# Optimization experiments

Hardware: AMD Instinct MI355X
Metric: run time of the kernel (lower is better)

## Reference

```python
import jax, jax.numpy as jnp
import numpy as np

N, N1, N2, E, DIN, H = 100000, 60000, 30000, 1600000, 128, 64


def setup_inputs() -> dict:
    key = jax.random.key(0)
    ks = jax.random.split(key, 16)
    s = 0.05
    return {
        "feats0": jax.random.normal(ks[0], (N, DIN), jnp.float32),
        "feats1": jax.random.normal(ks[1], (N1, DIN), jnp.float32),
        "feats2": jax.random.normal(ks[2], (N2, DIN), jnp.float32),
        "mask_feat": jax.random.normal(ks[3], (N, DIN), jnp.float32),
        "src1": jax.random.randint(ks[4], (E,), 0, N, jnp.int32),
        "dst1": jax.random.randint(ks[5], (E,), 0, N1, jnp.int32),
        "src2": jax.random.randint(ks[6], (E,), 0, N, jnp.int32),
        "dst2": jax.random.randint(ks[7], (E,), 0, N2, jnp.int32),
        "W0": jax.random.normal(ks[8], (DIN, H), jnp.float32) * s,
        "b0": jnp.zeros((H,), jnp.float32),
        "W1": jax.random.normal(ks[9], (DIN, H), jnp.float32) * s,
        "b1": jnp.zeros((H,), jnp.float32),
        "W2": jax.random.normal(ks[10], (DIN, H), jnp.float32) * s,
        "b2": jnp.zeros((H,), jnp.float32),
        "A0": jax.random.normal(ks[11], (H, H), jnp.float32) * s,
        "A1": jax.random.normal(ks[12], (H, H), jnp.float32) * s,
    }


def _mean_agg(h_nei, src, dst, num_tar):
    # sparse mm(nei_index, h_nei) / count  ==  degree-normalized neighbor mean
    summed = jax.ops.segment_sum(h_nei[dst], src, num_segments=num_tar)
    cnt = jax.ops.segment_sum(jnp.ones(src.shape, h_nei.dtype), src, num_segments=num_tar)
    cnt = jnp.where(cnt > 0, cnt, 1.0)[:, None]  # torch.where(count>0, count, 1)
    return summed / cnt


def reference(feats0, feats1, feats2, mask_feat, src1, dst1, src2, dst2,
              W0, b0, W1, b1, W2, b2, A0, A1):
    elu = jax.nn.elu
    h_tar = elu(feats0 @ W0 + b0)
    h_mask = elu(mask_feat @ W0 + b0)
    h_nei1 = elu(feats1 @ W1 + b1)
    h_nei2 = elu(feats2 @ W2 + b2)

    agg1 = _mean_agg(h_nei1, src1, dst1, feats0.shape[0]) @ A0
    agg2 = _mean_agg(h_nei2, src2, dst2, feats0.shape[0]) @ A1

    view1 = elu(h_tar + agg1)
    mask1 = elu(h_mask + agg1)
    view2 = elu(h_tar + agg2)
    mask2 = elu(h_mask + agg2)
    # [5, N, H]: per-relation view/mask embeddings plus coarse target embedding
    return jnp.stack([view1, mask1, view2, mask2, h_tar])
```

## Files before the change

kernel.cpp:

```cpp
#include <hip/hip_runtime.h>
#include <hip/hip_bf16.h>


typedef short  bf16x8 __attribute__((ext_vector_type(8)));
typedef float  f32x4  __attribute__((ext_vector_type(4)));
typedef int    i32x4  __attribute__((ext_vector_type(4)));

#define MFMA_BF16(a, b, c) __builtin_amdgcn_mfma_f32_16x16x32_bf16((a), (b), (c), 0, 0, 0)

__device__ __forceinline__ ushort f2bf(float f) {
  return (ushort)((__float_as_uint(f) + 0x8000u) >> 16);
}
__device__ __forceinline__ float eluf(float x) {
  return x > 0.f ? x : (__expf(x) - 1.f);
}
__device__ __forceinline__ bf16x8 cvt8(const float* __restrict__ p) {
  f32x4 lo = *(const f32x4*)p;
  f32x4 hi = *(const f32x4*)(p + 4);
  union { unsigned u[4]; bf16x8 v; } r;
#pragma unroll
  for (int j = 0; j < 2; ++j) {
    unsigned a = __float_as_uint(lo[2 * j])     + 0x8000u;
    unsigned b = __float_as_uint(lo[2 * j + 1]) + 0x8000u;
    r.u[j] = (a >> 16) | (b & 0xFFFF0000u);
    unsigned c = __float_as_uint(hi[2 * j])     + 0x8000u;
    unsigned d = __float_as_uint(hi[2 * j + 1]) + 0x8000u;
    r.u[2 + j] = (c >> 16) | (d & 0xFFFF0000u);
  }
  return r.v;
}

__global__ __launch_bounds__(256) void pack_frags_kernel(
    const float* __restrict__ W0, const float* __restrict__ W1,
    const float* __restrict__ W2, const float* __restrict__ A0,
    const float* __restrict__ A1, ushort* __restrict__ out) {
  int gw   = (blockIdx.x * blockDim.x + threadIdx.x) >> 6;
  int lane = threadIdx.x & 63;
  if (gw >= 64) return;
  const float* src; ushort* dst; int f;
  if (gw < 16)      { src = W0; dst = out;         f = gw;      }
  else if (gw < 32) { src = W1; dst = out + 8192;  f = gw - 16; }
  else if (gw < 48) { src = W2; dst = out + 16384; f = gw - 32; }
  else if (gw < 56) { src = A0; dst = out + 24576; f = gw - 48; }
  else              { src = A1; dst = out + 28672; f = gw - 56; }
  int kc = f >> 2, ct = f & 3;
  int q = lane >> 4, c = lane & 15;
  ushort* d = dst + ((size_t)f * 64 + lane) * 8;
#pragma unroll
  for (int i = 0; i < 8; ++i)
    d[i] = f2bf(src[(kc * 32 + q * 8 + i) * 64 + ct * 16 + c]);
}

template <bool HASA>
__global__ __launch_bounds__(256) void lin_elu_kernel(
    const float* __restrict__ X, const ushort* __restrict__ Wp,
    const float* __restrict__ bias, const ushort* __restrict__ Ap,
    float* __restrict__ Y, int Mtiles) {
  __shared__ ushort plds[4][16 * 72];
  int lane  = threadIdx.x & 63;
  int q     = lane >> 4, c = lane & 15;
  int wslot = threadIdx.x >> 6;
  int wid   = blockIdx.x * 4 + wslot;
  int nw    = gridDim.x * 4;

  bf16x8 bw[4][4];
#pragma unroll
  for (int kc = 0; kc < 4; ++kc)
#pragma unroll
    for (int ct = 0; ct < 4; ++ct)
      bw[kc][ct] = *(const bf16x8*)(Wp + (((kc << 2) | ct) * 64 + lane) * 8);

  float bv[4];
#pragma unroll
  for (int ct = 0; ct < 4; ++ct) bv[ct] = bias[ct * 16 + c];

  bf16x8 ba[2][4];
  if (HASA) {
#pragma unroll
    for (int kc = 0; kc < 2; ++kc)
#pragma unroll
      for (int ct = 0; ct < 4; ++ct)
        ba[kc][ct] = *(const bf16x8*)(Ap + (((kc << 2) | ct) * 64 + lane) * 8);
  }

  ushort* myp = plds[wslot];

  for (int t = wid; t < Mtiles; t += nw) {
    const float* xr = X + ((size_t)(t * 16 + c)) * 128 + q * 8;
    bf16x8 a0 = cvt8(xr);
    bf16x8 a1 = cvt8(xr + 32);
    bf16x8 a2 = cvt8(xr + 64);
    bf16x8 a3 = cvt8(xr + 96);

    f32x4 acc[4];
#pragma unroll
    for (int ct = 0; ct < 4; ++ct) {
      f32x4 a = {0.f, 0.f, 0.f, 0.f};
      a = MFMA_BF16(a0, bw[0][ct], a);
      a = MFMA_BF16(a1, bw[1][ct], a);
      a = MFMA_BF16(a2, bw[2][ct], a);
      a = MFMA_BF16(a3, bw[3][ct], a);
      acc[ct] = a;
    }

    float* yr = Y + ((size_t)t * 16) * 64;
    if (!HASA) {
#pragma unroll
      for (int ct = 0; ct < 4; ++ct)
#pragma unroll
        for (int r = 0; r < 4; ++r)
          yr[(q * 4 + r) * 64 + ct * 16 + c] = eluf(acc[ct][r] + bv[ct]);
    } else {
#pragma unroll
      for (int ct = 0; ct < 4; ++ct)
#pragma unroll
        for (int r = 0; r < 4; ++r)
          myp[(q * 4 + r) * 72 + ct * 16 + c] = f2bf(eluf(acc[ct][r] + bv[ct]));
      bf16x8 p0 = *(const bf16x8*)(myp + c * 72 + q * 8);
      bf16x8 p1 = *(const bf16x8*)(myp + c * 72 + 32 + q * 8);
      f32x4 acc2[4];
#pragma unroll
      for (int ct = 0; ct < 4; ++ct) {
        f32x4 a = {0.f, 0.f, 0.f, 0.f};
        a = MFMA_BF16(p0, ba[0][ct], a);
        a = MFMA_BF16(p1, ba[1][ct], a);
        acc2[ct] = a;
      }
#pragma unroll
      for (int ct = 0; ct < 4; ++ct)
#pragma unroll
        for (int r = 0; r < 4; ++r)
          yr[(q * 4 + r) * 64 + ct * 16 + c] = acc2[ct][r];
    }
  }
}

__global__ __launch_bounds__(256) void bucket_count_kernel(
    const int* __restrict__ src1, const int* __restrict__ src2,
    int* __restrict__ btot, int E, int N) {
  __shared__ int h[256];
  int t = threadIdx.x;
  h[t] = 0;
  __syncthreads();
  int n4 = (2 * E) >> 2;
  int stride = gridDim.x * blockDim.x;
  for (int i = blockIdx.x * blockDim.x + t; i < n4; i += stride) {
    int e4 = i << 2;
    i32x4 k;
    if (e4 < E) k = *(const i32x4*)(src1 + e4);
    else {
      k = *(const i32x4*)(src2 + (e4 - E));
#pragma unroll
      for (int j = 0; j < 4; ++j) k[j] += N;
    }
#pragma unroll
    for (int j = 0; j < 4; ++j) atomicAdd(&h[k[j] >> 10], 1);
  }
  __syncthreads();
  if (h[t]) atomicAdd(&btot[t], h[t]);
}

__global__ __launch_bounds__(256) void bscan_kernel(
    const int* __restrict__ btot, int* __restrict__ bstart,
    int* __restrict__ bcur, int NB) {
  __shared__ int lds[256];
  int t = threadIdx.x;
  int v = (t < NB) ? btot[t] : 0;
  lds[t] = v; __syncthreads();
  for (int off = 1; off < 256; off <<= 1) {
    int x = lds[t];
    int a = (t >= off) ? lds[t - off] : 0;
    __syncthreads();
    lds[t] = x + a;
    __syncthreads();
  }
  int incl = lds[t];
  if (t < NB) { bstart[t] = incl - v; bcur[t] = incl - v; }
  if (t == NB - 1) bstart[NB] = incl;
}

#define P1_CHUNK 8192
__global__ __launch_bounds__(256) void partition_kernel(
    const int* __restrict__ src1, const int* __restrict__ dst1,
    const int* __restrict__ src2, const int* __restrict__ dst2,
    int* __restrict__ bcur, unsigned* __restrict__ pairs, int E, int N) {
  __shared__ int hist[256], sbuf[256], lbase[256], lcur[256], gstart[256];
  __shared__ unsigned img[P1_CHUNK];
  int t  = threadIdx.x;
  int M  = 2 * N;
  int NB = (M + 1023) >> 10;
  int cb = blockIdx.x * P1_CHUNK;
  int ng = (2 * E - cb) >> 2;
  if (ng > P1_CHUNK / 4) ng = P1_CHUNK / 4;

  hist[t] = 0;
  __syncthreads();

  for (int i = t; i < ng; i += 256) {
    int e4 = cb + (i << 2);
    i32x4 k;
    if (e4 < E) k = *(const i32x4*)(src1 + e4);
    else {
      k = *(const i32x4*)(src2 + (e4 - E));
#pragma unroll
      for (int j = 0; j < 4; ++j) k[j] += N;
    }
#pragma unroll
    for (int j = 0; j < 4; ++j) atomicAdd(&hist[k[j] >> 10], 1);
  }
  __syncthreads();

  sbuf[t] = hist[t];
  __syncthreads();
  for (int off = 1; off < 256; off <<= 1) {
    int x = sbuf[t];
    int a = (t >= off) ? sbuf[t - off] : 0;
    __syncthreads();
    sbuf[t] = x + a;
    __syncthreads();
  }
  lbase[t] = sbuf[t] - hist[t];
  lcur[t]  = sbuf[t] - hist[t];
  if (t < NB) gstart[t] = atomicAdd(&bcur[t], hist[t]);
  __syncthreads();

  for (int i = t; i < ng; i += 256) {
    int e4 = cb + (i << 2);
    i32x4 k, v;
    if (e4 < E) {
      k = *(const i32x4*)(src1 + e4);
      v = *(const i32x4*)(dst1 + e4);
    } else {
      k = *(const i32x4*)(src2 + (e4 - E));
      v = *(const i32x4*)(dst2 + (e4 - E));
#pragma unroll
      for (int j = 0; j < 4; ++j) k[j] += N;
    }
#pragma unroll
    for (int j = 0; j < 4; ++j) {
      int b  = k[j] >> 10;
      int lp = atomicAdd(&lcur[b], 1);
      img[lp] = ((unsigned)(k[j] & 1023) << 16) | (unsigned)v[j];
    }
  }
  __syncthreads();

  int w = t >> 6, lane = t & 63;
  for (int b = w; b < NB; b += 4) {
    int len = hist[b], lb = lbase[b], gs = gstart[b];
    for (int i = lane; i < len; i += 64)
      pairs[gs + i] = img[lb + i];
  }
}

#define P2_CAP 18432
__global__ __launch_bounds__(256) void scatter_kernel(
    const int* __restrict__ bstart, const unsigned* __restrict__ pairs,
    int* __restrict__ row_ptr, int* __restrict__ nbr, int M) {
  __shared__ int cur[1024];
  __shared__ int ssum[256];
  __shared__ int img[P2_CAP];
  int t     = threadIdx.x;
  int b     = blockIdx.x;
  int kbase = b << 10;
  int kend  = kbase + 1024; if (kend > M) kend = M;
  int kcnt  = kend - kbase;
  int pbase = bstart[b];
  int cnt   = bstart[b + 1] - pbase;

#pragma unroll
  for (int j = 0; j < 4; ++j) cur[t * 4 + j] = 0;
  __syncthreads();
  for (int i = t; i < cnt; i += 256)
    atomicAdd(&cur[pairs[pbase + i] >> 16], 1);
  __syncthreads();

  int c0 = cur[t * 4], c1 = cur[t * 4 + 1], c2 = cur[t * 4 + 2], c3 = cur[t * 4 + 3];
  int s  = c0 + c1 + c2 + c3;
  ssum[t] = s;
  __syncthreads();
  for (int off = 1; off < 256; off <<= 1) {
    int x = ssum[t];
    int a = (t >= off) ? ssum[t - off] : 0;
    __syncthreads();
    ssum[t] = x + a;
    __syncthreads();
  }
  int run = ssum[t] - s;
  int e0 = run, e1 = run + c0, e2 = e1 + c1, e3 = e2 + c2;
  cur[t * 4] = e0; cur[t * 4 + 1] = e1; cur[t * 4 + 2] = e2; cur[t * 4 + 3] = e3;
  if (t * 4 + 3 < kcnt) {
    i32x4 rp = { pbase + e0, pbase + e1, pbase + e2, pbase + e3 };
    *(i32x4*)(row_ptr + kbase + t * 4) = rp;
  } else {
    if (t * 4     < kcnt) row_ptr[kbase + t * 4]     = pbase + e0;
    if (t * 4 + 1 < kcnt) row_ptr[kbase + t * 4 + 1] = pbase + e1;
    if (t * 4 + 2 < kcnt) row_ptr[kbase + t * 4 + 2] = pbase + e2;
    if (t * 4 + 3 < kcnt) row_ptr[kbase + t * 4 + 3] = pbase + e3;
  }
  if (t == 0 && kend == M) row_ptr[M] = pbase + cnt;
  __syncthreads();

  for (int i = t; i < cnt; i += 256) {
    unsigned p = pairs[pbase + i];
    int kl = (int)(p >> 16);
    int v  = (int)(p & 0xFFFFu);
    int pos = atomicAdd(&cur[kl], 1);
    if (pos < P2_CAP) img[pos] = v;
    else              nbr[pbase + pos] = v;
  }
  __syncthreads();

  int lim = cnt < P2_CAP ? cnt : P2_CAP;
  for (int i = t; i < lim; i += 256) nbr[pbase + i] = img[i];
}

__global__ __launch_bounds__(256) void aggregate_kernel(
    const int* __restrict__ row_ptr, const int* __restrict__ nbr,
    const float* __restrict__ g1, const float* __restrict__ g2,
    float* __restrict__ avg1, float* __restrict__ avg2, int N) {
  int lane = threadIdx.x & 63;
  int v = blockIdx.x * 4 + (threadIdx.x >> 6);
  if (v >= 2 * N) return;
  int n0 = row_ptr[v], n1 = row_ptr[v + 1];
  const float* __restrict__ g = (v < N) ? g1 : g2;
  float acc = 0.f;
  for (int base = n0; base < n1; base += 64) {
    int rem = n1 - base;
    int m = rem < 64 ? rem : 64;
    int idx = (lane < m) ? nbr[base + lane] : 0;
    int j = 0;
    for (; j + 4 <= m; j += 4) {
      int d0 = __shfl(idx, j), d1 = __shfl(idx, j + 1);
      int d2 = __shfl(idx, j + 2), d3 = __shfl(idx, j + 3);
      float v0 = g[(size_t)d0 * 64 + lane];
      float v1 = g[(size_t)d1 * 64 + lane];
      float v2 = g[(size_t)d2 * 64 + lane];
      float v3 = g[(size_t)d3 * 64 + lane];
      acc += v0 + v1 + v2 + v3;
    }
    for (; j < m; ++j) {
      int d = __shfl(idx, j);
      acc += g[(size_t)d * 64 + lane];
    }
  }
  int deg = n1 - n0;
  float a = (deg > 0) ? acc / (float)deg : 0.f;
  if (v < N) avg1[(size_t)v * 64 + lane] = a;
  else       avg2[(size_t)(v - N) * 64 + lane] = a;
}

__global__ __launch_bounds__(256) void finalize_kernel(
    const float* __restrict__ avg1, const float* __restrict__ avg2,
    float* __restrict__ out, int N) {
  int i = blockIdx.x * blockDim.x + threadIdx.x;
  if (i >= N * 16) return;
  size_t base  = ((size_t)i) << 2;
  size_t plane = (size_t)N * 64;
  f32x4 t = *(const f32x4*)(out + 4 * plane + base);
  f32x4 m = *(const f32x4*)(out + plane + base);
  f32x4 a1 = *(const f32x4*)(avg1 + base);
  f32x4 a2 = *(const f32x4*)(avg2 + base);
  f32x4 v1, m1, v2, m2;
#pragma unroll
  for (int j = 0; j < 4; ++j) {
    v1[j] = eluf(t[j] + a1[j]);
    m1[j] = eluf(m[j] + a1[j]);
    v2[j] = eluf(t[j] + a2[j]);
    m2[j] = eluf(m[j] + a2[j]);
  }
  *(f32x4*)(out + base)             = v1;
  *(f32x4*)(out + plane + base)     = m1;
  *(f32x4*)(out + 2 * plane + base) = v2;
  *(f32x4*)(out + 3 * plane + base) = m2;
}

static inline int imin(int a, int b) { return a < b ? a : b; }

extern "C" void kernel_launch(void* const* d_in, const int* in_sizes, int n_in,
                              void* d_out, int out_size, void* d_ws, size_t ws_size,
                              hipStream_t stream) {
  const float* feats0 = (const float*)d_in[0];
  const float* feats1 = (const float*)d_in[1];
  const float* feats2 = (const float*)d_in[2];
  const float* maskf  = (const float*)d_in[3];
  const int* src1 = (const int*)d_in[4];
  const int* dst1 = (const int*)d_in[5];
  const int* src2 = (const int*)d_in[6];
  const int* dst2 = (const int*)d_in[7];
  const float* W0 = (const float*)d_in[8];
  const float* b0 = (const float*)d_in[9];
  const float* W1 = (const float*)d_in[10];
  const float* b1 = (const float*)d_in[11];
  const float* W2 = (const float*)d_in[12];
  const float* b2 = (const float*)d_in[13];
  const float* A0 = (const float*)d_in[14];
  const float* A1 = (const float*)d_in[15];

  int N  = in_sizes[0] / 128;
  int N1 = in_sizes[1] / 128;
  int N2 = in_sizes[2] / 128;
  int E  = in_sizes[4];
  int M  = 2 * N;

  float* out = (float*)d_out;
  size_t plane = (size_t)N * 64;
  float* h_tar  = out + 4 * plane;
  float* h_mask = out + plane;

  float* g1      = (float*)d_ws;
  float* g2      = g1 + (size_t)N1 * 64;
  float* avg1    = g2 + (size_t)N2 * 64;
  float* avg2    = avg1 + (size_t)N * 64;
  int*   row_ptr = (int*)(avg2 + (size_t)N * 64);
  int*   btot    = row_ptr + M + 1;
  int*   bstart  = btot + 256;
  int*   bcur    = bstart + 257;
  int*   nbr     = bcur + 256;
  unsigned* pairs = (unsigned*)(nbr + 2 * E);
  ushort* frags  = (ushort*)(pairs + 2 * E);

  hipMemsetAsync(btot, 0, 256 * sizeof(int), stream);

  pack_frags_kernel<<<16, 256, 0, stream>>>(W0, W1, W2, A0, A1, frags);

  int t0 = N / 16, t1 = N1 / 16, t2 = N2 / 16;
  lin_elu_kernel<false><<<imin(2048, (t0 + 3) / 4), 256, 0, stream>>>(
      feats0, frags, b0, nullptr, h_tar, t0);
  lin_elu_kernel<false><<<imin(2048, (t0 + 3) / 4), 256, 0, stream>>>(
      maskf, frags, b0, nullptr, h_mask, t0);
  lin_elu_kernel<true><<<imin(2048, (t1 + 3) / 4), 256, 0, stream>>>(
      feats1, frags + 8192, b1, frags + 24576, g1, t1);
  lin_elu_kernel<true><<<imin(2048, (t2 + 3) / 4), 256, 0, stream>>>(
      feats2, frags + 16384, b2, frags + 28672, g2, t2);

  int NB = (M + 1023) >> 10;
  bucket_count_kernel<<<512, 256, 0, stream>>>(src1, src2, btot, E, N);
  bscan_kernel<<<1, 256, 0, stream>>>(btot, bstart, bcur, NB);

  int p1blocks = (2 * E + P1_CHUNK - 1) / P1_CHUNK;
  partition_kernel<<<p1blocks, 256, 0, stream>>>(
      src1, dst1, src2, dst2, bcur, pairs, E, N);
  scatter_kernel<<<NB, 256, 0, stream>>>(bstart, pairs, row_ptr, nbr, M);

  aggregate_kernel<<<(M + 3) / 4, 256, 0, stream>>>(
      row_ptr, nbr, g1, g2, avg1, avg2, N);

  finalize_kernel<<<(N * 16 + 255) / 256, 256, 0, stream>>>(avg1, avg2, out, N);
}
```

Measured before the change: 512.2 us.

## Store projected neighbor features and averages in bf16 to halve gather traffic

The pre-projected neighbor tables g1/g2 and the per-node averages are now stored as bf16 instead of fp32. The aggregation kernel is reworked so each half-wave handles a different neighbor, with each lane reading two packed bf16 values. The halves are combined with a cross-lane shuffle before the averaged result is written back as bf16. This is meant to cut the bytes moved by the random-access gather and by the finalize pass, at the cost of extra rounding error in the aggregated embeddings. The workspace layout is also reordered.

```diff
diff --git a/kernel.cpp b/kernel.cpp
--- a/kernel.cpp
+++ b/kernel.cpp
@@ -14,6 +14,8 @@
 __device__ __forceinline__ float eluf(float x) {
   return x > 0.f ? x : (__expf(x) - 1.f);
 }
+__device__ __forceinline__ float bflo(unsigned u) { return __uint_as_float(u << 16); }
+__device__ __forceinline__ float bfhi(unsigned u) { return __uint_as_float(u & 0xFFFF0000u); }
 __device__ __forceinline__ bf16x8 cvt8(const float* __restrict__ p) {
   f32x4 lo = *(const f32x4*)p;
   f32x4 hi = *(const f32x4*)(p + 4);
@@ -55,7 +57,7 @@
 __global__ __launch_bounds__(256) void lin_elu_kernel(
     const float* __restrict__ X, const ushort* __restrict__ Wp,
     const float* __restrict__ bias, const ushort* __restrict__ Ap,
-    float* __restrict__ Y, int Mtiles) {
+    void* __restrict__ Yv, int Mtiles) {
   __shared__ ushort plds[4][16 * 72];
   int lane  = threadIdx.x & 63;
   int q     = lane >> 4, c = lane & 15;
@@ -103,8 +105,8 @@
       acc[ct] = a;
     }
 
-    float* yr = Y + ((size_t)t * 16) * 64;
     if (!HASA) {
+      float* yr = (float*)Yv + ((size_t)t * 16) * 64;
 #pragma unroll
       for (int ct = 0; ct < 4; ++ct)
 #pragma unroll
@@ -126,11 +128,12 @@
         a = MFMA_BF16(p1, ba[1][ct], a);
         acc2[ct] = a;
       }
+      ushort* yb = (ushort*)Yv + ((size_t)t * 16) * 64;
 #pragma unroll
       for (int ct = 0; ct < 4; ++ct)
 #pragma unroll
         for (int r = 0; r < 4; ++r)
-          yr[(q * 4 + r) * 64 + ct * 16 + c] = acc2[ct][r];
+          yb[(q * 4 + r) * 64 + ct * 16 + c] = f2bf(acc2[ct][r]);
     }
   }
 }
@@ -317,41 +320,54 @@
 
 __global__ __launch_bounds__(256) void aggregate_kernel(
     const int* __restrict__ row_ptr, const int* __restrict__ nbr,
-    const float* __restrict__ g1, const float* __restrict__ g2,
-    float* __restrict__ avg1, float* __restrict__ avg2, int N) {
+    const ushort* __restrict__ g1, const ushort* __restrict__ g2,
+    ushort* __restrict__ avg1, ushort* __restrict__ avg2, int N) {
   int lane = threadIdx.x & 63;
   int v = blockIdx.x * 4 + (threadIdx.x >> 6);
   if (v >= 2 * N) return;
   int n0 = row_ptr[v], n1 = row_ptr[v + 1];
-  const float* __restrict__ g = (v < N) ? g1 : g2;
-  float acc = 0.f;
+  const ushort* __restrict__ g = (v < N) ? g1 : g2;
+  int half = lane >> 5;
+  int c2   = (lane & 31) << 1;
+  float ax = 0.f, ay = 0.f;
   for (int base = n0; base < n1; base += 64) {
     int rem = n1 - base;
     int m = rem < 64 ? rem : 64;
     int idx = (lane < m) ? nbr[base + lane] : 0;
     int j = 0;
-    for (; j + 4 <= m; j += 4) {
-      int d0 = __shfl(idx, j), d1 = __shfl(idx, j + 1);
-      int d2 = __shfl(idx, j + 2), d3 = __shfl(idx, j + 3);
-      float v0 = g[(size_t)d0 * 64 + lane];
-      float v1 = g[(size_t)d1 * 64 + lane];
-      float v2 = g[(size_t)d2 * 64 + lane];
-      float v3 = g[(size_t)d3 * 64 + lane];
-      acc += v0 + v1 + v2 + v3;
-    }
-    for (; j < m; ++j) {
-      int d = __shfl(idx, j);
-      acc += g[(size_t)d * 64 + lane];
-    }
-  }
-  int deg = n1 - n0;
-  float a = (deg > 0) ? acc / (float)deg : 0.f;
-  if (v < N) avg1[(size_t)v * 64 + lane] = a;
-  else       avg2[(size_t)(v - N) * 64 + lane] = a;
+    for (; j + 8 <= m; j += 8) {
+      int d0 = __shfl(idx, j + half);
+      int d1 = __shfl(idx, j + 2 + half);
+      int d2 = __shfl(idx, j + 4 + half);
+      int d3 = __shfl(idx, j + 6 + half);
+      unsigned u0 = *(const unsigned*)(g + (size_t)d0 * 64 + c2);
+      unsigned u1 = *(const unsigned*)(g + (size_t)d1 * 64 + c2);
+      unsigned u2 = *(const unsigned*)(g + (size_t)d2 * 64 + c2);
+      unsigned u3 = *(const unsigned*)(g + (size_t)d3 * 64 + c2);
+      ax += bflo(u0) + bflo(u1) + bflo(u2) + bflo(u3);
+      ay += bfhi(u0) + bfhi(u1) + bfhi(u2) + bfhi(u3);
+    }
+    for (; j < m; j += 2) {
+      int jj = j + half;
+      int d = __shfl(idx, jj);
+      unsigned u = *(const unsigned*)(g + (size_t)d * 64 + c2);
+      if (jj < m) { ax += bflo(u); ay += bfhi(u); }
+    }
+  }
+  ax += __shfl_xor(ax, 32);
+  ay += __shfl_xor(ay, 32);
+  if (lane < 32) {
+    int deg = n1 - n0;
+    float s = (deg > 0) ? 1.f / (float)deg : 0.f;
+    unsigned w = (unsigned)f2bf(ax * s) | ((unsigned)f2bf(ay * s) << 16);
+    ushort* av = (v < N) ? avg1 : avg2;
+    int vv = (v < N) ? v : v - N;
+    *(unsigned*)(av + (size_t)vv * 64 + c2) = w;
+  }
 }
 
 __global__ __launch_bounds__(256) void finalize_kernel(
-    const float* __restrict__ avg1, const float* __restrict__ avg2,
+    const ushort* __restrict__ avg1, const ushort* __restrict__ avg2,
     float* __restrict__ out, int N) {
   int i = blockIdx.x * blockDim.x + threadIdx.x;
   if (i >= N * 16) return;
@@ -359,8 +375,12 @@
   size_t plane = (size_t)N * 64;
   f32x4 t = *(const f32x4*)(out + 4 * plane + base);
   f32x4 m = *(const f32x4*)(out + plane + base);
-  f32x4 a1 = *(const f32x4*)(avg1 + base);
-  f32x4 a2 = *(const f32x4*)(avg2 + base);
+  unsigned a1l = *(const unsigned*)(avg1 + base);
+  unsigned a1h = *(const unsigned*)(avg1 + base + 2);
+  unsigned a2l = *(const unsigned*)(avg2 + base);
+  unsigned a2h = *(const unsigned*)(avg2 + base + 2);
+  float a1[4] = { bflo(a1l), bfhi(a1l), bflo(a1h), bfhi(a1h) };
+  float a2[4] = { bflo(a2l), bfhi(a2l), bflo(a2h), bfhi(a2h) };
   f32x4 v1, m1, v2, m2;
 #pragma unroll
   for (int j = 0; j < 4; ++j) {
@@ -408,17 +428,17 @@
   float* h_tar  = out + 4 * plane;
   float* h_mask = out + plane;
 
-  float* g1      = (float*)d_ws;
-  float* g2      = g1 + (size_t)N1 * 64;
-  float* avg1    = g2 + (size_t)N2 * 64;
-  float* avg2    = avg1 + (size_t)N * 64;
-  int*   row_ptr = (int*)(avg2 + (size_t)N * 64);
-  int*   btot    = row_ptr + M + 1;
-  int*   bstart  = btot + 256;
-  int*   bcur    = bstart + 257;
-  int*   nbr     = bcur + 256;
+  ushort* frags  = (ushort*)d_ws;
+  int* row_ptr   = (int*)((char*)d_ws + 65536);
+  int* btot      = row_ptr + M + 1;
+  int* bstart    = btot + 256;
+  int* bcur      = bstart + 257;
+  int* nbr       = bcur + 256;
   unsigned* pairs = (unsigned*)(nbr + 2 * E);
-  ushort* frags  = (ushort*)(pairs + 2 * E);
+  ushort* g1b    = (ushort*)(pairs + 2 * E);
+  ushort* g2b    = g1b + (size_t)N1 * 64;
+  ushort* avg1b  = g2b + (size_t)N2 * 64;
+  ushort* avg2b  = avg1b + (size_t)N * 64;
 
   hipMemsetAsync(btot, 0, 256 * sizeof(int), stream);
 
@@ -430,9 +450,9 @@
   lin_elu_kernel<false><<<imin(2048, (t0 + 3) / 4), 256, 0, stream>>>(
       maskf, frags, b0, nullptr, h_mask, t0);
   lin_elu_kernel<true><<<imin(2048, (t1 + 3) / 4), 256, 0, stream>>>(
-      feats1, frags + 8192, b1, frags + 24576, g1, t1);
+      feats1, frags + 8192, b1, frags + 24576, g1b, t1);
   lin_elu_kernel<true><<<imin(2048, (t2 + 3) / 4), 256, 0, stream>>>(
-      feats2, frags + 16384, b2, frags + 28672, g2, t2);
+      feats2, frags + 16384, b2, frags + 28672, g2b, t2);
 
   int NB = (M + 1023) >> 10;
   bucket_count_kernel<<<512, 256, 0, stream>>>(src1, src2, btot, E, N);
@@ -444,7 +464,7 @@
   scatter_kernel<<<NB, 256, 0, stream>>>(bstart, pairs, row_ptr, nbr, M);
 
   aggregate_kernel<<<(M + 3) / 4, 256, 0, stream>>>(
-      row_ptr, nbr, g1, g2, avg1, avg2, N);
-
-  finalize_kernel<<<(N * 16 + 255) / 256, 256, 0, stream>>>(avg1, avg2, out, N);
-}
+      row_ptr, nbr, g1b, g2b, avg1b, avg2b, N);
+
+  finalize_kernel<<<(N * 16 + 255) / 256, 256, 0, stream>>>(avg1b, avg2b, out, N);
+}
```

After: 484.1 us. -5.5%, faster.
